# Performance work log

Measured on AMD Instinct MI355X. Metric: run time of the kernel, lower is better.

## Reference

```python
import jax, jax.numpy as jnp
import numpy as np

SLOPE = 25.0  # snntorch surrogate.fast_sigmoid default slope

@jax.custom_vjp
def fast_sigmoid(x):
    # Forward: Heaviside step (spike); backward: fast-sigmoid surrogate grad.
    return (x > 0).astype(x.dtype)

def _fs_fwd(x):
    return fast_sigmoid(x), x

def _fs_bwd(x, g):
    return (g / (SLOPE * jnp.abs(x) + 1.0) ** 2,)

fast_sigmoid.defvjp(_fs_fwd, _fs_bwd)


def setup_inputs() -> dict:
    key = jax.random.key(0)
    k0, k1, k2, k3, k4 = jax.random.split(key, 5)
    B, IN, OUT, T = 512, 512, 512, 64
    x = jax.random.normal(k0, (B, IN), jnp.float32)
    W = jax.random.normal(k1, (OUT, IN), jnp.float32) / np.sqrt(IN).astype(np.float32)
    b = jnp.zeros((OUT,), jnp.float32)
    # learnable scalars (0.0 in source init; small nonzero to exercise the P recurrence)
    alpha = jax.random.uniform(k2, (1,), jnp.float32) * 0.1
    eta = jax.random.uniform(k3, (1,), jnp.float32) * 0.01
    beta = jax.random.uniform(k4, (1,), jnp.float32) * 0.1
    P0 = jnp.zeros((OUT, IN), jnp.float32)
    return {"x": x, "W": W, "b": b, "alpha": alpha, "eta": eta, "beta": beta, "P0": P0, "T": T}


def reference(x, W, b, alpha, eta, beta, P0, T):
    # x: [B, IN], W: [OUT, IN], P0: [OUT, IN]
    tao_u, tao_w, dt, V_th = 5.0, 1.0, 1.0, 0.2
    k = jnp.float32(dt / tao_u)
    a = alpha.reshape(())
    e = eta.reshape(())
    bt = beta.reshape(())
    # MLP output is constant across timesteps (same s_batch each step)
    mlp_T = jax.nn.relu(x @ W.T + b).T  # [OUT, B]
    xT = x.T  # [IN, B]
    decay_p = jnp.exp(jnp.float32(-dt / tao_w))

    # NOTE: reset() zeroes u and s every step, so only P is recurrent:
    # u_m = k * (mlp_out * exp(-m/tao_w) + alpha * P @ x^T)
    def step(P, m):
        u = k * (mlp_T * jnp.exp(-m / tao_w) + a * (P @ xT))  # [OUT, B]
        P_new = P * decay_p + e * ((fast_sigmoid(u) + bt) @ x)  # [OUT, IN]
        s = fast_sigmoid(u - V_th)  # [OUT, B]
        return P_new, s.T  # emit [B, OUT]

    _, spk = jax.lax.scan(step, P0, jnp.arange(T, dtype=jnp.float32))
    return spk  # [T, B, OUT]
```

## Files before the change

### kernel.cpp

```cpp
#include <hip/hip_runtime.h>


#define NN 512

__global__ __launch_bounds__(256) void gemm_splitk_kernel(
    const float* __restrict__ x, const float* __restrict__ W,
    const float* __restrict__ P0, float* __restrict__ part)
{
    const int tid = threadIdx.x;
    const int bid = blockIdx.x;
    const int out = bid >> 8;
    const int rem = bid & 255;
    const int kq = rem >> 6;
    const int tl = rem & 63;
    const int rb = (tl >> 3) << 6;
    const int cb = (tl & 7) << 6;
    const int kbase = kq << 7;

    const float* A = ((out == 0) ? W : (out == 1) ? P0 : x) + (size_t)rb * NN;
    const float* Bx = x + (size_t)cb * NN;
    float* D = part + (size_t)(out * 4 + kq) * NN * NN;

    const int tx = tid & 15;
    const int ty = tid >> 4;

    __shared__ float At[32][68];
    __shared__ float Bt[32][68];

    const int lr = tid >> 2;
    const int lk = (tid & 3) << 3;

    float acc[4][4] = {{0.f,0.f,0.f,0.f},{0.f,0.f,0.f,0.f},
                       {0.f,0.f,0.f,0.f},{0.f,0.f,0.f,0.f}};

    float4 a0 = *(const float4*)(A + (size_t)lr * NN + kbase + lk);
    float4 a1 = *(const float4*)(A + (size_t)lr * NN + kbase + lk + 4);
    float4 b0 = *(const float4*)(Bx + (size_t)lr * NN + kbase + lk);
    float4 b1 = *(const float4*)(Bx + (size_t)lr * NN + kbase + lk + 4);

    for (int c = 0; c < 4; ++c) {
        __syncthreads();
        At[lk + 0][lr] = a0.x; At[lk + 1][lr] = a0.y;
        At[lk + 2][lr] = a0.z; At[lk + 3][lr] = a0.w;
        At[lk + 4][lr] = a1.x; At[lk + 5][lr] = a1.y;
        At[lk + 6][lr] = a1.z; At[lk + 7][lr] = a1.w;
        Bt[lk + 0][lr] = b0.x; Bt[lk + 1][lr] = b0.y;
        Bt[lk + 2][lr] = b0.z; Bt[lk + 3][lr] = b0.w;
        Bt[lk + 4][lr] = b1.x; Bt[lk + 5][lr] = b1.y;
        Bt[lk + 6][lr] = b1.z; Bt[lk + 7][lr] = b1.w;
        __syncthreads();

        if (c < 3) {
            const int k0 = kbase + ((c + 1) << 5);
            a0 = *(const float4*)(A + (size_t)lr * NN + k0 + lk);
            a1 = *(const float4*)(A + (size_t)lr * NN + k0 + lk + 4);
            b0 = *(const float4*)(Bx + (size_t)lr * NN + k0 + lk);
            b1 = *(const float4*)(Bx + (size_t)lr * NN + k0 + lk + 4);
        }

#pragma unroll
        for (int k = 0; k < 32; ++k) {
            const float4 av = *(const float4*)&At[k][4 * ty];
            const float4 bv = *(const float4*)&Bt[k][4 * tx];
            const float avs[4] = {av.x, av.y, av.z, av.w};
            const float bvs[4] = {bv.x, bv.y, bv.z, bv.w};
#pragma unroll
            for (int i = 0; i < 4; ++i)
#pragma unroll
                for (int j = 0; j < 4; ++j)
                    acc[i][j] = fmaf(avs[i], bvs[j], acc[i][j]);
        }
    }

#pragma unroll
    for (int i = 0; i < 4; ++i) {
        const int r = rb + 4 * ty + i;
        *(float4*)(D + (size_t)r * NN + cb + 4 * tx) =
            make_float4(acc[i][0], acc[i][1], acc[i][2], acc[i][3]);
    }
}

__global__ __launch_bounds__(256) void combine_kernel(
    const float* __restrict__ part, const float* __restrict__ bias,
    float* __restrict__ M, float* __restrict__ V0, float* __restrict__ G)
{
    const int idx = blockIdx.x * 256 + threadIdx.x;
    const int out = idx >> 16;
    const int io = idx & 65535;
    const float4* p = (const float4*)(part + (size_t)out * 4 * NN * NN);
    const float4 p0 = p[io];
    const float4 p1 = p[io + 65536];
    const float4 p2 = p[io + 131072];
    const float4 p3 = p[io + 196608];
    float4 s;
    s.x = (p0.x + p1.x) + (p2.x + p3.x);
    s.y = (p0.y + p1.y) + (p2.y + p3.y);
    s.z = (p0.z + p1.z) + (p2.z + p3.z);
    s.w = (p0.w + p1.w) + (p2.w + p3.w);
    if (out == 0) {
        const float bb = bias[io >> 7];
        s.x = fmaxf(s.x + bb, 0.f); s.y = fmaxf(s.y + bb, 0.f);
        s.z = fmaxf(s.z + bb, 0.f); s.w = fmaxf(s.w + bb, 0.f);
        ((float4*)M)[io] = s;
    } else if (out == 1) {
        ((float4*)V0)[io] = s;
    } else {
        ((float4*)G)[io] = s;
    }
}

__global__ __launch_bounds__(256) void acc0cs_kernel(
    const float* __restrict__ M, const float* __restrict__ V0,
    const float* __restrict__ G, const float* __restrict__ alpha,
    float* __restrict__ ACC0, float* __restrict__ gs)
{
    const int tid = threadIdx.x;
    const int rb = (blockIdx.x >> 4) << 5;
    const int cb = (blockIdx.x & 15) << 5;
    const float a = alpha[0];
    const float kk = 0.2f;

    __shared__ float Ht[32][36];
    __shared__ float Bt[32][36];

    const int tx = tid & 15;
    const int ty = tid >> 4;
    const int lr = tid >> 3;
    const int lk = (tid & 7) << 2;

    float acc[2][2] = {{0.f, 0.f}, {0.f, 0.f}};

    for (int k0 = 0; k0 < NN; k0 += 32) {
        const float4 mv = *(const float4*)(M + (size_t)(rb + lr) * NN + k0 + lk);
        const float4 vv = *(const float4*)(V0 + (size_t)(rb + lr) * NN + k0 + lk);
        const float4 gv = *(const float4*)(G + (size_t)(k0 + lr) * NN + cb + lk);
        __syncthreads();
        Ht[lk + 0][lr] = (kk * fmaf(a, vv.x, mv.x) > 0.f) ? 1.f : 0.f;
        Ht[lk + 1][lr] = (kk * fmaf(a, vv.y, mv.y) > 0.f) ? 1.f : 0.f;
        Ht[lk + 2][lr] = (kk * fmaf(a, vv.z, mv.z) > 0.f) ? 1.f : 0.f;
        Ht[lk + 3][lr] = (kk * fmaf(a, vv.w, mv.w) > 0.f) ? 1.f : 0.f;
        Bt[lr][lk + 0] = gv.x; Bt[lr][lk + 1] = gv.y;
        Bt[lr][lk + 2] = gv.z; Bt[lr][lk + 3] = gv.w;
        __syncthreads();

#pragma unroll
        for (int k = 0; k < 32; ++k) {
            const float2 av = *(const float2*)&Ht[k][2 * ty];
            const float2 bv = *(const float2*)&Bt[k][2 * tx];
            acc[0][0] = fmaf(av.x, bv.x, acc[0][0]);
            acc[0][1] = fmaf(av.x, bv.y, acc[0][1]);
            acc[1][0] = fmaf(av.y, bv.x, acc[1][0]);
            acc[1][1] = fmaf(av.y, bv.y, acc[1][1]);
        }
    }

#pragma unroll
    for (int i = 0; i < 2; ++i) {
        *(float2*)(ACC0 + (size_t)(rb + 2 * ty + i) * NN + cb + 2 * tx) =
            make_float2(acc[i][0], acc[i][1]);
    }

    if (rb == 0) {
        __syncthreads();
        float* red = (float*)Ht;
        const int c = cb + (tid & 31);
        const int g = tid >> 5;
        float s = 0.f;
#pragma unroll 8
        for (int bp = 64 * g; bp < 64 * g + 64; ++bp)
            s += G[(size_t)bp * NN + c];
        red[g * 32 + (tid & 31)] = s;
        __syncthreads();
        if (g == 0) {
            const int cc = tid & 31;
            const float tot =
                ((red[cc] + red[32 + cc]) + (red[64 + cc] + red[96 + cc])) +
                ((red[128 + cc] + red[160 + cc]) + (red[192 + cc] + red[224 + cc]));
            gs[c] = tot;
        }
    }
}

__global__ __launch_bounds__(512, 4) void snn_bits7_kernel(
    const float* __restrict__ M, const float* __restrict__ G,
    const float* __restrict__ V0, const float* __restrict__ ACC0,
    const float* __restrict__ gs, const float* __restrict__ alpha,
    const float* __restrict__ eta, const float* __restrict__ beta,
    unsigned* __restrict__ sp, int T)
{
    const int tid = threadIdx.x;
    const int w = tid >> 6;
    const int lane = tid & 63;
    const int r = blockIdx.x;

    __shared__ unsigned long long lflag[2];
    __shared__ int wcnt[8];
    __shared__ unsigned short list[528] __attribute__((aligned(16)));

    const float a = alpha[0], e = eta[0], bt = beta[0];
    const float kk = 0.2f;
    const float dd = 0.36787944117144233f;
    const float Vth = 0.2f;

    const size_t rc = (size_t)r * NN + tid;
    const float m = M[rc];
    float v = V0[rc];
    const float cg = e * bt * gs[tid];
    const float* Gc = G + tid;

    float acc;
    float em;
    unsigned long long oldw;

    {
        const float u = kk * fmaf(a, v, m * 1.0f);
        const unsigned long long hb = __ballot(u > 0.f);
        const unsigned long long sb = __ballot(u > Vth);
        if (lane == 0)
            *(unsigned long long*)(sp + (size_t)r * 16 + 2 * w) = sb;
        oldw = hb;
        acc = ACC0[rc];
        v = fmaf(dd, v, fmaf(e, acc, cg));
        em = dd;
    }

    for (int t = 1; t < T; ++t) {
        const float u = kk * fmaf(a, v, m * em);
        const unsigned long long hb = __ballot(u > 0.f);
        const unsigned long long sb = __ballot(u > Vth);
        const unsigned long long xw = hb ^ oldw;
        const int p = t & 1;
        if (lane == 0) {
            ((unsigned char*)&lflag[p])[w] = (xw != 0ull) ? (unsigned char)1 : (unsigned char)0;
            wcnt[w] = (int)__popcll(xw);
            *(unsigned long long*)(sp + ((size_t)t * NN + r) * 16 + 2 * w) = sb;
        }
        __syncthreads();

        if (lflag[p] != 0ull) {
            const int c0 = wcnt[0], c1 = wcnt[1], c2 = wcnt[2], c3 = wcnt[3];
            const int c4 = wcnt[4], c5 = wcnt[5], c6 = wcnt[6], c7 = wcnt[7];
            const int ntot = ((c0 + c1) + (c2 + c3)) + ((c4 + c5) + (c6 + c7));
            int base = 0;
            if (w > 0) base += c0;
            if (w > 1) base += c1;
            if (w > 2) base += c2;
            if (w > 3) base += c3;
            if (w > 4) base += c4;
            if (w > 5) base += c5;
            if (w > 6) base += c6;

            if ((xw >> lane) & 1ull) {
                const int pos = (int)__popcll(xw & ((1ull << lane) - 1ull));
                const unsigned row = (unsigned)((w << 6) + lane);
                const unsigned sgn = (unsigned)((hb >> lane) & 1ull) << 15;
                list[base + pos] = (unsigned short)(row | sgn);
            }
            __syncthreads();

            float s0 = 0.f, s1 = 0.f, s2 = 0.f, s3 = 0.f;
            float s4 = 0.f, s5 = 0.f, s6 = 0.f, s7 = 0.f;
            for (int j = 0; j < ntot; j += 8) {
                const uint4 le = *(const uint4*)(list + j);
                const unsigned e0 = le.x & 0xFFFFu, e1 = le.x >> 16;
                const unsigned e2 = le.y & 0xFFFFu, e3 = le.y >> 16;
                const unsigned e4 = le.z & 0xFFFFu, e5 = le.z >> 16;
                const unsigned e6 = le.w & 0xFFFFu, e7 = le.w >> 16;
                const float g0 = Gc[(size_t)(e0 & 511u) << 9];
                const float g1 = Gc[(size_t)(e1 & 511u) << 9];
                const float g2 = Gc[(size_t)(e2 & 511u) << 9];
                const float g3 = Gc[(size_t)(e3 & 511u) << 9];
                const float g4 = Gc[(size_t)(e4 & 511u) << 9];
                const float g5 = Gc[(size_t)(e5 & 511u) << 9];
                const float g6 = Gc[(size_t)(e6 & 511u) << 9];
                const float g7 = Gc[(size_t)(e7 & 511u) << 9];
                s0 += (j + 0 < ntot) ? ((e0 & 0x8000u) ? g0 : -g0) : 0.0f;
                s1 += (j + 1 < ntot) ? ((e1 & 0x8000u) ? g1 : -g1) : 0.0f;
                s2 += (j + 2 < ntot) ? ((e2 & 0x8000u) ? g2 : -g2) : 0.0f;
                s3 += (j + 3 < ntot) ? ((e3 & 0x8000u) ? g3 : -g3) : 0.0f;
                s4 += (j + 4 < ntot) ? ((e4 & 0x8000u) ? g4 : -g4) : 0.0f;
                s5 += (j + 5 < ntot) ? ((e5 & 0x8000u) ? g5 : -g5) : 0.0f;
                s6 += (j + 6 < ntot) ? ((e6 & 0x8000u) ? g6 : -g6) : 0.0f;
                s7 += (j + 7 < ntot) ? ((e7 & 0x8000u) ? g7 : -g7) : 0.0f;
            }
            acc += ((s0 + s1) + (s2 + s3)) + ((s4 + s5) + (s6 + s7));
        }

        oldw = hb;
        v = fmaf(dd, v, fmaf(e, acc, cg));
        em *= dd;
    }
}

__global__ __launch_bounds__(256) void expand_kernel(
    const unsigned* __restrict__ sp, float* __restrict__ out)
{
    const int tid = threadIdx.x;
    const int t = blockIdx.x >> 3;
    const int bt8 = blockIdx.x & 7;

    __shared__ uint2 sh[NN];
    const uint2* spw = (const uint2*)sp;
    sh[tid]       = spw[((size_t)t * NN + tid) * 8 + bt8];
    sh[tid + 256] = spw[((size_t)t * NN + tid + 256) * 8 + bt8];
    __syncthreads();

    const int b = bt8 * 64 + (tid >> 2);
    const int sub = tid & 3;
    const int rw = (tid >> 2) >> 5;
    const int bit = b & 31;
    float* op = out + (size_t)t * (NN * NN) + (size_t)b * NN;

#pragma unroll 4
    for (int i = 0; i < 32; ++i) {
        const int o = sub * 4 + i * 16;
        const uint2 w0 = sh[o];
        const uint2 w1 = sh[o + 1];
        const uint2 w2 = sh[o + 2];
        const uint2 w3 = sh[o + 3];
        float4 f;
        f.x = (float)(((rw ? w0.y : w0.x) >> bit) & 1u);
        f.y = (float)(((rw ? w1.y : w1.x) >> bit) & 1u);
        f.z = (float)(((rw ? w2.y : w2.x) >> bit) & 1u);
        f.w = (float)(((rw ? w3.y : w3.x) >> bit) & 1u);
        *(float4*)(op + o) = f;
    }
}

__global__ __launch_bounds__(256) void gemm64_kernel(
    const float* __restrict__ x, const float* __restrict__ W,
    const float* __restrict__ P0, const float* __restrict__ bias,
    float* __restrict__ M, float* __restrict__ V0, float* __restrict__ G)
{
    const int tid = threadIdx.x;
    const int bid = blockIdx.x;
    const int out = bid >> 6;
    const int tl = bid & 63;
    const int rb = (tl >> 3) << 6;
    const int cb = (tl & 7) << 6;

    const float* A = ((out == 0) ? W : (out == 1) ? P0 : x) + (size_t)rb * NN;
    const float* Bx = x + (size_t)cb * NN;
    float* D = (out == 0) ? M : (out == 1) ? V0 : G;

    const int tx = tid & 15;
    const int ty = tid >> 4;

    __shared__ float At[32][68];
    __shared__ float Bt[32][68];

    const int lr = tid >> 2;
    const int lk = (tid & 3) << 3;

    float acc[4][4] = {{0.f,0.f,0.f,0.f},{0.f,0.f,0.f,0.f},
                       {0.f,0.f,0.f,0.f},{0.f,0.f,0.f,0.f}};

    float4 a0 = *(const float4*)(A + (size_t)lr * NN + lk);
    float4 a1 = *(const float4*)(A + (size_t)lr * NN + lk + 4);
    float4 b0 = *(const float4*)(Bx + (size_t)lr * NN + lk);
    float4 b1 = *(const float4*)(Bx + (size_t)lr * NN + lk + 4);

    for (int c = 0; c < 16; ++c) {
        __syncthreads();
        At[lk + 0][lr] = a0.x; At[lk + 1][lr] = a0.y;
        At[lk + 2][lr] = a0.z; At[lk + 3][lr] = a0.w;
        At[lk + 4][lr] = a1.x; At[lk + 5][lr] = a1.y;
        At[lk + 6][lr] = a1.z; At[lk + 7][lr] = a1.w;
        Bt[lk + 0][lr] = b0.x; Bt[lk + 1][lr] = b0.y;
        Bt[lk + 2][lr] = b0.z; Bt[lk + 3][lr] = b0.w;
        Bt[lk + 4][lr] = b1.x; Bt[lk + 5][lr] = b1.y;
        Bt[lk + 6][lr] = b1.z; Bt[lk + 7][lr] = b1.w;
        __syncthreads();

        if (c < 15) {
            const int k0 = (c + 1) << 5;
            a0 = *(const float4*)(A + (size_t)lr * NN + k0 + lk);
            a1 = *(const float4*)(A + (size_t)lr * NN + k0 + lk + 4);
            b0 = *(const float4*)(Bx + (size_t)lr * NN + k0 + lk);
            b1 = *(const float4*)(Bx + (size_t)lr * NN + k0 + lk + 4);
        }

#pragma unroll
        for (int k = 0; k < 32; ++k) {
            const float4 av = *(const float4*)&At[k][4 * ty];
            const float4 bv = *(const float4*)&Bt[k][4 * tx];
            const float avs[4] = {av.x, av.y, av.z, av.w};
            const float bvs[4] = {bv.x, bv.y, bv.z, bv.w};
#pragma unroll
            for (int i = 0; i < 4; ++i)
#pragma unroll
                for (int j = 0; j < 4; ++j)
                    acc[i][j] = fmaf(avs[i], bvs[j], acc[i][j]);
        }
    }

#pragma unroll
    for (int i = 0; i < 4; ++i) {
        const int r = rb + 4 * ty + i;
        float4 o = make_float4(acc[i][0], acc[i][1], acc[i][2], acc[i][3]);
        if (out == 0) {
            const float bb = bias[r];
            o.x = fmaxf(o.x + bb, 0.f); o.y = fmaxf(o.y + bb, 0.f);
            o.z = fmaxf(o.z + bb, 0.f); o.w = fmaxf(o.w + bb, 0.f);
        }
        *(float4*)(D + (size_t)r * NN + cb + 4 * tx) = o;
    }
}

__global__ __launch_bounds__(256) void colsum_kernel(
    const float* __restrict__ G, float* __restrict__ gs)
{
    __shared__ float red[4][64];
    const int tid = threadIdx.x;
    const int c = (blockIdx.x << 6) + (tid & 63);
    const int g = tid >> 6;
    float s = 0.f;
#pragma unroll 8
    for (int bp = 128 * g; bp < 128 * g + 128; ++bp) s += G[(size_t)bp * NN + c];
    if (g > 0) red[g][tid & 63] = s;
    __syncthreads();
    if (g == 0) gs[c] = ((s + red[1][tid & 63]) + red[2][tid & 63]) + red[3][tid & 63];
}

__global__ __launch_bounds__(256) void snn_step_kernel(
    const float* __restrict__ M, const float* __restrict__ G,
    const float* __restrict__ V0, const float* __restrict__ gs,
    const float* __restrict__ alpha, const float* __restrict__ eta,
    const float* __restrict__ beta, float* __restrict__ out, int T)
{
    const int j = threadIdx.x;
    const int r0 = blockIdx.x * 2;
    const int c0 = 2 * j;
    const float a = alpha[0], e = eta[0], bt = beta[0];
    const float kk = 0.2f, dd = 0.36787944117144233f, Vth = 0.2f;

    float v00 = V0[r0 * NN + c0];
    float v01 = V0[r0 * NN + c0 + 1];
    float v10 = V0[(r0 + 1) * NN + c0];
    float v11 = V0[(r0 + 1) * NN + c0 + 1];
    const float m00 = M[r0 * NN + c0];
    const float m01 = M[r0 * NN + c0 + 1];
    const float m10 = M[(r0 + 1) * NN + c0];
    const float m11 = M[(r0 + 1) * NN + c0 + 1];
    const float gs0 = gs[c0];
    const float gs1 = gs[c0 + 1];

    __shared__ float2 hp[NN];
    float em = 1.0f;
    const float2* Gcol = (const float2*)G + j;

    for (int t = 0; t < T; ++t) {
        const float u00 = kk * (m00 * em + a * v00);
        const float u01 = kk * (m01 * em + a * v01);
        const float u10 = kk * (m10 * em + a * v10);
        const float u11 = kk * (m11 * em + a * v11);

        float* outp = out + (size_t)t * (NN * NN);
        float2 sA = make_float2(u00 > Vth ? 1.f : 0.f, u10 > Vth ? 1.f : 0.f);
        float2 sB = make_float2(u01 > Vth ? 1.f : 0.f, u11 > Vth ? 1.f : 0.f);
        *(float2*)(outp + (size_t)c0 * NN + r0) = sA;
        *(float2*)(outp + (size_t)(c0 + 1) * NN + r0) = sB;

        hp[c0]     = make_float2(u00 > 0.f ? 1.f : 0.f, u10 > 0.f ? 1.f : 0.f);
        hp[c0 + 1] = make_float2(u01 > 0.f ? 1.f : 0.f, u11 > 0.f ? 1.f : 0.f);
        __syncthreads();

        float acc00 = 0.f, acc01 = 0.f, acc10 = 0.f, acc11 = 0.f;
#pragma unroll 8
        for (int bp = 0; bp < NN; ++bp) {
            float2 h = hp[bp];
            float2 g = Gcol[(size_t)bp * 256];
            acc00 = fmaf(h.x, g.x, acc00);
            acc01 = fmaf(h.x, g.y, acc01);
            acc10 = fmaf(h.y, g.x, acc10);
            acc11 = fmaf(h.y, g.y, acc11);
        }

        v00 = dd * v00 + e * (acc00 + bt * gs0);
        v01 = dd * v01 + e * (acc01 + bt * gs1);
        v10 = dd * v10 + e * (acc10 + bt * gs0);
        v11 = dd * v11 + e * (acc11 + bt * gs1);
        em *= dd;
        __syncthreads();
    }
}

extern "C" void kernel_launch(void* const* d_in, const int* in_sizes, int n_in,
                              void* d_out, int out_size, void* d_ws, size_t ws_size,
                              hipStream_t stream)
{
    const float* x     = (const float*)d_in[0];
    const float* W     = (const float*)d_in[1];
    const float* bias  = (const float*)d_in[2];
    const float* alpha = (const float*)d_in[3];
    const float* eta   = (const float*)d_in[4];
    const float* beta  = (const float*)d_in[5];
    const float* P0    = (const float*)d_in[6];
    (void)in_sizes; (void)n_in;

    const int T = out_size / (NN * NN);

    float* ws   = (float*)d_ws;
    float* part = ws;
    float* M    = ws + 12 * NN * NN;
    float* V0   = ws + 13 * NN * NN;
    float* G    = ws + 14 * NN * NN;
    float* ACC0 = ws + 15 * NN * NN;
    float* gsv  = ws + 16 * NN * NN;
    unsigned* sp = (unsigned*)(gsv + NN);

    const size_t need_main = ((size_t)16 * NN * NN + NN) * 4 + (size_t)T * NN * 16 * 4;

    if (ws_size >= need_main) {
        hipLaunchKernelGGL(gemm_splitk_kernel, dim3(768), dim3(256), 0, stream,
                           x, W, P0, part);
        hipLaunchKernelGGL(combine_kernel, dim3(768), dim3(256), 0, stream,
                           part, bias, M, V0, G);
        hipLaunchKernelGGL(acc0cs_kernel, dim3(256), dim3(256), 0, stream,
                           M, V0, G, alpha, ACC0, gsv);
        hipLaunchKernelGGL(snn_bits7_kernel, dim3(NN), dim3(512), 0, stream,
                           M, G, V0, ACC0, gsv, alpha, eta, beta, sp, T);
        hipLaunchKernelGGL(expand_kernel, dim3(T * 8), dim3(256), 0, stream,
                           sp, (float*)d_out);
    } else {
        float* Mf  = ws;
        float* V0f = ws + NN * NN;
        float* Gf  = ws + 2 * NN * NN;
        float* gs2 = ws + 3 * NN * NN;
        hipLaunchKernelGGL(gemm64_kernel, dim3(192), dim3(256), 0, stream,
                           x, W, P0, bias, Mf, V0f, Gf);
        hipLaunchKernelGGL(colsum_kernel, dim3(8), dim3(256), 0, stream, Gf, gs2);
        hipLaunchKernelGGL(snn_step_kernel, dim3(256), dim3(256), 0, stream,
                           Mf, Gf, V0f, gs2, alpha, eta, beta, (float*)d_out, T);
    }
}
```

Before: 116.4 us.

## Split-K the ACC0 GEMM and add certified early exit for converged rows

The initial spike-by-G product is now an 8-way split-K GEMM with 64x64 tiles and a 4x4 register microtile, writing partial sums that the recurrence kernel adds up at startup. The column-sum of G is split the same way. In the recurrence kernel, when no Heaviside bit flips in a step, a per-row test checks whether every element's trajectory toward its fixed point keeps the same sign. If it does, the remaining steps run as a closed-form affine update with no list building or G gathers. This skips most of the per-step work for rows that have settled, but it relies on a tolerance-based sign argument that may not hold exactly in floating point.

```diff
diff --git a/kernel.cpp b/kernel.cpp
--- a/kernel.cpp
+++ b/kernel.cpp
@@ -109,82 +109,113 @@
     }
 }
 
-__global__ __launch_bounds__(256) void acc0cs_kernel(
+__global__ __launch_bounds__(256) void acc0_splitk_kernel(
     const float* __restrict__ M, const float* __restrict__ V0,
     const float* __restrict__ G, const float* __restrict__ alpha,
-    float* __restrict__ ACC0, float* __restrict__ gs)
+    float* __restrict__ ACC0p, float* __restrict__ gsp)
 {
     const int tid = threadIdx.x;
-    const int rb = (blockIdx.x >> 4) << 5;
-    const int cb = (blockIdx.x & 15) << 5;
+    const int bid = blockIdx.x;
+    const int kq = bid >> 6;
+    const int tl = bid & 63;
+    const int rb = (tl >> 3) << 6;
+    const int cb = (tl & 7) << 6;
+    const int kbase = kq << 6;
+
     const float a = alpha[0];
     const float kk = 0.2f;
 
-    __shared__ float Ht[32][36];
-    __shared__ float Bt[32][36];
-
     const int tx = tid & 15;
     const int ty = tid >> 4;
-    const int lr = tid >> 3;
-    const int lk = (tid & 7) << 2;
-
-    float acc[2][2] = {{0.f, 0.f}, {0.f, 0.f}};
-
-    for (int k0 = 0; k0 < NN; k0 += 32) {
-        const float4 mv = *(const float4*)(M + (size_t)(rb + lr) * NN + k0 + lk);
-        const float4 vv = *(const float4*)(V0 + (size_t)(rb + lr) * NN + k0 + lk);
-        const float4 gv = *(const float4*)(G + (size_t)(k0 + lr) * NN + cb + lk);
-        __syncthreads();
-        Ht[lk + 0][lr] = (kk * fmaf(a, vv.x, mv.x) > 0.f) ? 1.f : 0.f;
-        Ht[lk + 1][lr] = (kk * fmaf(a, vv.y, mv.y) > 0.f) ? 1.f : 0.f;
-        Ht[lk + 2][lr] = (kk * fmaf(a, vv.z, mv.z) > 0.f) ? 1.f : 0.f;
-        Ht[lk + 3][lr] = (kk * fmaf(a, vv.w, mv.w) > 0.f) ? 1.f : 0.f;
-        Bt[lr][lk + 0] = gv.x; Bt[lr][lk + 1] = gv.y;
-        Bt[lr][lk + 2] = gv.z; Bt[lr][lk + 3] = gv.w;
-        __syncthreads();
+
+    __shared__ float At[32][68];
+    __shared__ float Bt[32][68];
+
+    const int ar = tid >> 2;
+    const int akk = (tid & 3) << 3;
+    const int kb = tid >> 3;
+    const int cl = (tid & 7) << 3;
+
+    float acc[4][4] = {{0.f,0.f,0.f,0.f},{0.f,0.f,0.f,0.f},
+                       {0.f,0.f,0.f,0.f},{0.f,0.f,0.f,0.f}};
+
+    float4 m0 = *(const float4*)(M + (size_t)(rb + ar) * NN + kbase + akk);
+    float4 m1 = *(const float4*)(M + (size_t)(rb + ar) * NN + kbase + akk + 4);
+    float4 v0 = *(const float4*)(V0 + (size_t)(rb + ar) * NN + kbase + akk);
+    float4 v1 = *(const float4*)(V0 + (size_t)(rb + ar) * NN + kbase + akk + 4);
+    float4 g0 = *(const float4*)(G + (size_t)(kbase + kb) * NN + cb + cl);
+    float4 g1 = *(const float4*)(G + (size_t)(kbase + kb) * NN + cb + cl + 4);
+
+    for (int c = 0; c < 2; ++c) {
+        __syncthreads();
+        At[akk + 0][ar] = (kk * fmaf(a, v0.x, m0.x) > 0.f) ? 1.f : 0.f;
+        At[akk + 1][ar] = (kk * fmaf(a, v0.y, m0.y) > 0.f) ? 1.f : 0.f;
+        At[akk + 2][ar] = (kk * fmaf(a, v0.z, m0.z) > 0.f) ? 1.f : 0.f;
+        At[akk + 3][ar] = (kk * fmaf(a, v0.w, m0.w) > 0.f) ? 1.f : 0.f;
+        At[akk + 4][ar] = (kk * fmaf(a, v1.x, m1.x) > 0.f) ? 1.f : 0.f;
+        At[akk + 5][ar] = (kk * fmaf(a, v1.y, m1.y) > 0.f) ? 1.f : 0.f;
+        At[akk + 6][ar] = (kk * fmaf(a, v1.z, m1.z) > 0.f) ? 1.f : 0.f;
+        At[akk + 7][ar] = (kk * fmaf(a, v1.w, m1.w) > 0.f) ? 1.f : 0.f;
+        Bt[kb][cl + 0] = g0.x; Bt[kb][cl + 1] = g0.y;
+        Bt[kb][cl + 2] = g0.z; Bt[kb][cl + 3] = g0.w;
+        Bt[kb][cl + 4] = g1.x; Bt[kb][cl + 5] = g1.y;
+        Bt[kb][cl + 6] = g1.z; Bt[kb][cl + 7] = g1.w;
+        __syncthreads();
+
+        if (c < 1) {
+            const int k0 = kbase + 32;
+            m0 = *(const float4*)(M + (size_t)(rb + ar) * NN + k0 + akk);
+            m1 = *(const float4*)(M + (size_t)(rb + ar) * NN + k0 + akk + 4);
+            v0 = *(const float4*)(V0 + (size_t)(rb + ar) * NN + k0 + akk);
+            v1 = *(const float4*)(V0 + (size_t)(rb + ar) * NN + k0 + akk + 4);
+            g0 = *(const float4*)(G + (size_t)(k0 + kb) * NN + cb + cl);
+            g1 = *(const float4*)(G + (size_t)(k0 + kb) * NN + cb + cl + 4);
+        }
 
 #pragma unroll
         for (int k = 0; k < 32; ++k) {
-            const float2 av = *(const float2*)&Ht[k][2 * ty];
-            const float2 bv = *(const float2*)&Bt[k][2 * tx];
-            acc[0][0] = fmaf(av.x, bv.x, acc[0][0]);
-            acc[0][1] = fmaf(av.x, bv.y, acc[0][1]);
-            acc[1][0] = fmaf(av.y, bv.x, acc[1][0]);
-            acc[1][1] = fmaf(av.y, bv.y, acc[1][1]);
-        }
-    }
-
-#pragma unroll
-    for (int i = 0; i < 2; ++i) {
-        *(float2*)(ACC0 + (size_t)(rb + 2 * ty + i) * NN + cb + 2 * tx) =
-            make_float2(acc[i][0], acc[i][1]);
-    }
-
-    if (rb == 0) {
-        __syncthreads();
-        float* red = (float*)Ht;
-        const int c = cb + (tid & 31);
-        const int g = tid >> 5;
+            const float4 av = *(const float4*)&At[k][4 * ty];
+            const float4 bv = *(const float4*)&Bt[k][4 * tx];
+            const float avs[4] = {av.x, av.y, av.z, av.w};
+            const float bvs[4] = {bv.x, bv.y, bv.z, bv.w};
+#pragma unroll
+            for (int i = 0; i < 4; ++i)
+#pragma unroll
+                for (int j = 0; j < 4; ++j)
+                    acc[i][j] = fmaf(avs[i], bvs[j], acc[i][j]);
+        }
+    }
+
+    float* Dp = ACC0p + (size_t)kq * NN * NN;
+#pragma unroll
+    for (int i = 0; i < 4; ++i) {
+        *(float4*)(Dp + (size_t)(rb + 4 * ty + i) * NN + cb + 4 * tx) =
+            make_float4(acc[i][0], acc[i][1], acc[i][2], acc[i][3]);
+    }
+
+    if ((tl >> 3) == 0) {
+        __syncthreads();
+        float* red = &At[0][0];
+        const int c = cb + (tid & 63);
+        const int g = tid >> 6;
         float s = 0.f;
-#pragma unroll 8
-        for (int bp = 64 * g; bp < 64 * g + 64; ++bp)
-            s += G[(size_t)bp * NN + c];
-        red[g * 32 + (tid & 31)] = s;
+#pragma unroll 16
+        for (int i = 0; i < 16; ++i)
+            s += G[(size_t)(kbase + 16 * g + i) * NN + c];
+        red[g * 64 + (tid & 63)] = s;
         __syncthreads();
         if (g == 0) {
-            const int cc = tid & 31;
-            const float tot =
-                ((red[cc] + red[32 + cc]) + (red[64 + cc] + red[96 + cc])) +
-                ((red[128 + cc] + red[160 + cc]) + (red[192 + cc] + red[224 + cc]));
-            gs[c] = tot;
-        }
-    }
-}
-
-__global__ __launch_bounds__(512, 4) void snn_bits7_kernel(
+            const int cc = tid & 63;
+            gsp[kq * NN + c] =
+                (red[cc] + red[64 + cc]) + (red[128 + cc] + red[192 + cc]);
+        }
+    }
+}
+
+__global__ __launch_bounds__(512, 4) void snn_bits9_kernel(
     const float* __restrict__ M, const float* __restrict__ G,
-    const float* __restrict__ V0, const float* __restrict__ ACC0,
-    const float* __restrict__ gs, const float* __restrict__ alpha,
+    const float* __restrict__ V0, const float* __restrict__ ACC0p,
+    const float* __restrict__ gsp, const float* __restrict__ alpha,
     const float* __restrict__ eta, const float* __restrict__ beta,
     unsigned* __restrict__ sp, int T)
 {
@@ -194,6 +225,7 @@
     const int r = blockIdx.x;
 
     __shared__ unsigned long long lflag[2];
+    __shared__ unsigned long long certf[2];
     __shared__ int wcnt[8];
     __shared__ unsigned short list[528] __attribute__((aligned(16)));
 
@@ -205,7 +237,10 @@
     const size_t rc = (size_t)r * NN + tid;
     const float m = M[rc];
     float v = V0[rc];
-    const float cg = e * bt * gs[tid];
+    const float gsum =
+        ((gsp[tid] + gsp[NN + tid]) + (gsp[2 * NN + tid] + gsp[3 * NN + tid])) +
+        ((gsp[4 * NN + tid] + gsp[5 * NN + tid]) + (gsp[6 * NN + tid] + gsp[7 * NN + tid]));
+    const float cg = e * bt * gsum;
     const float* Gc = G + tid;
 
     float acc;
@@ -219,7 +254,10 @@
         if (lane == 0)
             *(unsigned long long*)(sp + (size_t)r * 16 + 2 * w) = sb;
         oldw = hb;
-        acc = ACC0[rc];
+        const float* A0 = ACC0p + rc;
+        const size_t S = (size_t)NN * NN;
+        acc = ((A0[0] + A0[S]) + (A0[2 * S] + A0[3 * S]))
+            + ((A0[4 * S] + A0[5 * S]) + (A0[6 * S] + A0[7 * S]));
         v = fmaf(dd, v, fmaf(e, acc, cg));
         em = dd;
     }
@@ -237,6 +275,7 @@
         }
         __syncthreads();
 
+        bool certified = false;
         if (lflag[p] != 0ull) {
             const int c0 = wcnt[0], c1 = wcnt[1], c2 = wcnt[2], c3 = wcnt[3];
             const int c4 = wcnt[4], c5 = wcnt[5], c6 = wcnt[6], c7 = wcnt[7];
@@ -284,11 +323,38 @@
                 s7 += (j + 7 < ntot) ? ((e7 & 0x8000u) ? g7 : -g7) : 0.0f;
             }
             acc += ((s0 + s1) + (s2 + s3)) + ((s4 + s5) + (s6 + s7));
+        } else {
+            const float K0 = fmaf(e, acc, cg);
+            const float Vinf = K0 / (1.0f - dd);
+            const float uInf = kk * (a * Vinf);
+            const float C = u - uInf;
+            const bool okT = ((uInf > 0.f) == (u > 0.f)) &&
+                (fabsf(uInf) > fmaf(dd, fabsf(C),
+                                    1e-4f * (fabsf(uInf) + fabsf(C)) + 1e-12f));
+            const unsigned long long okm = __ballot(okT);
+            if (lane == 0)
+                ((unsigned char*)&certf[p])[w] =
+                    (okm == 0xFFFFFFFFFFFFFFFFull) ? (unsigned char)1 : (unsigned char)0;
+            __syncthreads();
+            certified = (certf[p] == 0x0101010101010101ull);
         }
 
         oldw = hb;
         v = fmaf(dd, v, fmaf(e, acc, cg));
         em *= dd;
+
+        if (certified) {
+            const float K = fmaf(e, acc, cg);
+            for (int t2 = t + 1; t2 < T; ++t2) {
+                const float u2 = kk * fmaf(a, v, m * em);
+                const unsigned long long sb2 = __ballot(u2 > Vth);
+                if (lane == 0)
+                    *(unsigned long long*)(sp + ((size_t)t2 * NN + r) * 16 + 2 * w) = sb2;
+                v = fmaf(dd, v, K);
+                em *= dd;
+            }
+            return;
+        }
     }
 }
 
@@ -500,26 +566,27 @@
 
     const int T = out_size / (NN * NN);
 
-    float* ws   = (float*)d_ws;
-    float* part = ws;
-    float* M    = ws + 12 * NN * NN;
-    float* V0   = ws + 13 * NN * NN;
-    float* G    = ws + 14 * NN * NN;
-    float* ACC0 = ws + 15 * NN * NN;
-    float* gsv  = ws + 16 * NN * NN;
-    unsigned* sp = (unsigned*)(gsv + NN);
-
-    const size_t need_main = ((size_t)16 * NN * NN + NN) * 4 + (size_t)T * NN * 16 * 4;
+    float* ws    = (float*)d_ws;
+    float* part  = ws;
+    float* ACC0p = ws;
+    float* M     = ws + 12 * NN * NN;
+    float* V0    = ws + 13 * NN * NN;
+    float* G     = ws + 14 * NN * NN;
+    float* gsp   = ws + 15 * NN * NN;
+    unsigned* sp = (unsigned*)(gsp + 8 * NN);
+
+    const size_t need_main = ((size_t)15 * NN * NN + 8 * NN) * 4
+                             + (size_t)T * NN * 16 * 4;
 
     if (ws_size >= need_main) {
         hipLaunchKernelGGL(gemm_splitk_kernel, dim3(768), dim3(256), 0, stream,
                            x, W, P0, part);
         hipLaunchKernelGGL(combine_kernel, dim3(768), dim3(256), 0, stream,
                            part, bias, M, V0, G);
-        hipLaunchKernelGGL(acc0cs_kernel, dim3(256), dim3(256), 0, stream,
-                           M, V0, G, alpha, ACC0, gsv);
-        hipLaunchKernelGGL(snn_bits7_kernel, dim3(NN), dim3(512), 0, stream,
-                           M, G, V0, ACC0, gsv, alpha, eta, beta, sp, T);
+        hipLaunchKernelGGL(acc0_splitk_kernel, dim3(512), dim3(256), 0, stream,
+                           M, V0, G, alpha, ACC0p, gsp);
+        hipLaunchKernelGGL(snn_bits9_kernel, dim3(NN), dim3(512), 0, stream,
+                           M, G, V0, ACC0p, gsp, alpha, eta, beta, sp, T);
         hipLaunchKernelGGL(expand_kernel, dim3(T * 8), dim3(256), 0, stream,
                            sp, (float*)d_out);
     } else {
```

After: 109.6 us. 5.8% less time.
